# Kernel tuning notes

Measured on AMD Instinct MI355X. Metric: run time of the kernel, lower is better.

The kernel has to match this reference:

```python
import jax, jax.numpy as jnp
import numpy as np

B, T, L, W = 4, 4096, 64, 8          # batch, text len, media tokens, max_window_per_audio
DIM, DIM_A, H, DH = 2048, 1024, 8, 64
INNER = H * DH
LN_EPS = 1e-5


def setup_inputs() -> dict:
    key = jax.random.key(0)
    ks = jax.random.split(key, 8)
    x = jax.random.normal(ks[0], (B, T, DIM), jnp.float32)
    media = jax.random.normal(ks[1], (B, L, 1, DIM_A), jnp.float32)
    media_mask = jax.random.uniform(ks[2], (B, L, 1)) > 0.1
    # sparse media markers (~8 per row); ensure at least one per row
    media_locations = (jax.random.uniform(ks[3], (B, T)) < (8.0 / T)).astype(jnp.int32)
    media_locations = media_locations.at[:, 0].set(1)
    Wq = jax.random.normal(ks[4], (DIM, INNER), jnp.float32) / np.sqrt(DIM).astype(np.float32)
    Wkv = jax.random.normal(ks[5], (DIM_A, 2 * INNER), jnp.float32) / np.sqrt(DIM_A).astype(np.float32)
    Wout = jax.random.normal(ks[6], (INNER, DIM), jnp.float32) / np.sqrt(INNER).astype(np.float32)
    gamma = jnp.ones((DIM,), jnp.float32)
    beta = jnp.zeros((DIM,), jnp.float32)
    return dict(x=x, media=media, media_mask=media_mask, media_locations=media_locations,
                Wq=Wq, Wkv=Wkv, Wout=Wout, gamma=gamma, beta=beta)


def reference(x, media, media_mask, media_locations, Wq, Wkv, Wout, gamma, beta):
    scale = DH ** -0.5
    # LayerNorm (biased variance, like torch)
    mu = x.mean(-1, keepdims=True)
    var = x.var(-1, keepdims=True)
    xn = (x - mu) * jax.lax.rsqrt(var + LN_EPS) * gamma + beta
    # projections
    q = (xn @ Wq).reshape(B, T, H, DH).transpose(0, 2, 1, 3) * scale   # [B,h,T,dh]
    kv = media.reshape(B, L, DIM_A) @ Wkv
    k, v = jnp.split(kv, 2, axis=-1)
    k = k.reshape(B, L, H, DH).transpose(0, 2, 1, 3)                   # [B,h,L,dh]
    v = v.reshape(B, L, H, DH).transpose(0, 2, 1, 3)
    sim = jnp.einsum('bhid,bhjd->bhij', q, k)                          # [B,h,T,L]
    big = jnp.finfo(sim.dtype).max
    # media validity mask
    mm = media_mask.reshape(B, 1, 1, L)
    sim = jnp.where(mm, sim, -big)
    # few-shot window mask (only_attend_immediate_media=False):
    # token t attends windows [0, max(#media at <=t, 1) * W)
    cum = jnp.cumsum((media_locations != 0).astype(jnp.int32), axis=1)  # [B,T]
    end = jnp.maximum(cum, 1) * W                                       # [B,T]
    fsm = jnp.arange(L)[None, None, :] < end[:, :, None]                # [B,T,L]
    sim = jnp.where(fsm[:, None], sim, -big)
    sim = sim - jax.lax.stop_gradient(sim.max(-1, keepdims=True))
    attn = jax.nn.softmax(sim, axis=-1)
    out = jnp.einsum('bhij,bhjd->bhid', attn, v)                        # [B,h,T,dh]
    out = out.transpose(0, 2, 1, 3).reshape(B, T, INNER)
    return out @ Wout
```

## Files before the change

kernel.cpp:

```cpp
#include <hip/hip_runtime.h>
#include <float.h>

typedef __bf16 bf16;
typedef __bf16 bf16x8 __attribute__((ext_vector_type(8)));
typedef float f32x4 __attribute__((ext_vector_type(4)));
typedef float f32x16 __attribute__((ext_vector_type(16)));

#define GAS __attribute__((address_space(1)))
#define LAS __attribute__((address_space(3)))

__device__ __forceinline__ void gload_lds16(const void* g, void* l) {
  __builtin_amdgcn_global_load_lds((const GAS unsigned int*)g, (LAS unsigned int*)l, 16, 0, 0);
}

template <int OUT_BF16>
__global__ __launch_bounds__(512, 2) void gemm_big(
    const bf16* __restrict__ A, const bf16* __restrict__ Bt,
    void* __restrict__ Cv, int M, int N, int K) {
  __shared__ __align__(16) bf16 Abuf[3][256 * 64];
  __shared__ __align__(16) bf16 Bbuf[3][128 * 64];
  const int tid = threadIdx.x, lane = tid & 63;
  const int w = tid >> 6, wr = w >> 2, wc = w & 3;
  const int l31 = lane & 31, hi = lane >> 5;

  const int gx = gridDim.x;
  const int nwg = gx * gridDim.y;
  int lid = blockIdx.y * gx + blockIdx.x;
  {
    const int qq = nwg >> 3, rr = nwg & 7;
    const int xcd = lid & 7, pos = lid >> 3;
    lid = (xcd < rr ? xcd * (qq + 1) : rr * (qq + 1) + (xcd - rr) * qq) + pos;
  }
  const int bx = lid % gx, by = lid / gx;
  const size_t m0 = (size_t)by * 256, n0 = (size_t)bx * 128;

  const int nt = K >> 6;
  const int srow = tid >> 3;
  const int sslot = tid & 7;

  f32x16 acc[4] = {};

  auto stage = [&](int t) {
    const int s = t % 3;
    const int kt = t << 6;
#pragma unroll
    for (int c = 0; c < 4; ++c) {
      const int r = c * 64 + srow;
      gload_lds16(A + (m0 + r) * (size_t)K + kt + ((sslot ^ (r & 7)) << 3),
                  &Abuf[s][c * 4096 + w * 512]);
    }
#pragma unroll
    for (int c = 0; c < 2; ++c) {
      const int r = c * 64 + srow;
      gload_lds16(Bt + (n0 + r) * (size_t)K + kt + ((sslot ^ (r & 7)) << 3),
                  &Bbuf[s][c * 4096 + w * 512]);
    }
  };

  auto rdA = [&](int s, int mi, int ks) {
    const int r = wr * 128 + mi * 32 + l31;
    return *(const bf16x8*)&Abuf[s][r * 64 + ((((ks << 1) | hi) ^ (r & 7)) << 3)];
  };
  auto rdB = [&](int s, int ks) {
    const int r = wc * 32 + l31;
    return *(const bf16x8*)&Bbuf[s][r * 64 + ((((ks << 1) | hi) ^ (r & 7)) << 3)];
  };

  auto compute = [&](int t) {
    const int s = t % 3;
    bf16x8 bv[4];
#pragma unroll
    for (int ks = 0; ks < 4; ++ks) bv[ks] = rdB(s, ks);
    __builtin_amdgcn_s_setprio(1);
#pragma unroll
    for (int ks = 0; ks < 4; ++ks)
#pragma unroll
      for (int mi = 0; mi < 4; ++mi) {
        const bf16x8 av = rdA(s, mi, ks);
        acc[mi] = __builtin_amdgcn_mfma_f32_32x32x16_bf16(av, bv[ks], acc[mi],
                                                          0, 0, 0);
      }
    __builtin_amdgcn_s_setprio(0);
  };

  stage(0);
  stage(1);

  for (int t = 0; t < nt - 1; ++t) {
    __builtin_amdgcn_sched_barrier(0);
    asm volatile("s_waitcnt vmcnt(6)" ::: "memory");
    __builtin_amdgcn_s_barrier();
    __builtin_amdgcn_sched_barrier(0);
    if (t + 2 < nt) stage(t + 2);
    compute(t);
  }
  __builtin_amdgcn_sched_barrier(0);
  asm volatile("s_waitcnt vmcnt(0)" ::: "memory");
  __builtin_amdgcn_s_barrier();
  __builtin_amdgcn_sched_barrier(0);
  compute(nt - 1);

#pragma unroll
  for (int mi = 0; mi < 4; ++mi)
#pragma unroll
    for (int rg = 0; rg < 16; ++rg) {
      const size_t row =
          m0 + wr * 128 + mi * 32 + (rg & 3) + ((rg >> 2) << 3) + (hi << 2);
      const size_t col = n0 + wc * 32 + l31;
      if (OUT_BF16)
        ((bf16*)Cv)[row * (size_t)N + col] = (bf16)acc[mi][rg];
      else
        ((float*)Cv)[row * (size_t)N + col] = acc[mi][rg];
    }
}

template <int OUT_BF16>
__global__ __launch_bounds__(256, 2) void gemm_bt(
    const bf16* __restrict__ A, const bf16* __restrict__ Bt,
    void* __restrict__ Cv, int M, int N, int K) {
  __shared__ bf16 As[128 * 32];
  __shared__ bf16 Bs[128 * 32];
  const int tid = threadIdx.x;
  const int lane = tid & 63, w = tid >> 6;
  const int wr = w >> 1, wc = w & 1;

  const int gx = gridDim.x;
  const int nwg = gx * gridDim.y;
  int lid = blockIdx.y * gx + blockIdx.x;
  {
    const int qq = nwg >> 3, rr = nwg & 7;
    const int xcd = lid & 7, pos = lid >> 3;
    lid = (xcd < rr ? xcd * (qq + 1) : rr * (qq + 1) + (xcd - rr) * qq) + pos;
  }
  const int bx = lid % gx, by = lid / gx;
  const size_t m0 = (size_t)by * 128, n0 = (size_t)bx * 128;

  const int srow = lane >> 2, sslot = lane & 3;
  const int g = lane >> 4, fr = lane & 15;

  f32x4 acc[4][4] = {};

  for (int kt = 0; kt < K; kt += 32) {
    __syncthreads();
#pragma unroll
    for (int j = 0; j < 2; ++j) {
      const int c = 2 * w + j;
      const int r = c * 16 + srow;
      const int ks = (sslot ^ (r & 3)) << 3;
      gload_lds16(A + (m0 + r) * K + kt + ks, &As[c * 512]);
      gload_lds16(Bt + (n0 + r) * K + kt + ks, &Bs[c * 512]);
    }
    __syncthreads();
    bf16x8 av[4], bv[4];
#pragma unroll
    for (int mi = 0; mi < 4; ++mi) {
      const int r = wr * 64 + mi * 16 + fr;
      av[mi] = *(const bf16x8*)&As[r * 32 + ((g ^ (r & 3)) << 3)];
    }
#pragma unroll
    for (int ni = 0; ni < 4; ++ni) {
      const int r = wc * 64 + ni * 16 + fr;
      bv[ni] = *(const bf16x8*)&Bs[r * 32 + ((g ^ (r & 3)) << 3)];
    }
#pragma unroll
    for (int mi = 0; mi < 4; ++mi)
#pragma unroll
      for (int ni = 0; ni < 4; ++ni)
        acc[mi][ni] = __builtin_amdgcn_mfma_f32_16x16x32_bf16(
            av[mi], bv[ni], acc[mi][ni], 0, 0, 0);
  }

#pragma unroll
  for (int mi = 0; mi < 4; ++mi)
#pragma unroll
    for (int ni = 0; ni < 4; ++ni)
#pragma unroll
      for (int rg = 0; rg < 4; ++rg) {
        const size_t row = m0 + wr * 64 + mi * 16 + g * 4 + rg;
        const size_t col = n0 + wc * 64 + ni * 16 + fr;
        if (OUT_BF16)
          ((bf16*)Cv)[row * (size_t)N + col] = (bf16)acc[mi][ni][rg];
        else
          ((float*)Cv)[row * (size_t)N + col] = acc[mi][ni][rg];
      }
}

__device__ __forceinline__ void transp64(const float* __restrict__ src,
                                         bf16* __restrict__ dst, int R, int C,
                                         float scale, int tile, float* lds) {
  const int tilesC = C >> 6;
  const int tr = tile / tilesC, tc = tile % tilesC;
  const int r0 = tr << 6, c0 = tc << 6;
  const int tid = threadIdx.x;
  const int lr = tid >> 6, lc = tid & 63;
#pragma unroll
  for (int j = 0; j < 16; ++j) {
    const int r = j * 4 + lr;
    lds[r * 65 + lc] = src[(size_t)(r0 + r) * C + c0 + lc];
  }
  __syncthreads();
#pragma unroll
  for (int j = 0; j < 16; ++j) {
    const int rr = j * 4 + lr;
    dst[(size_t)(c0 + rr) * R + r0 + lc] = (bf16)(lds[lc * 65 + rr] * scale);
  }
}

__global__ __launch_bounds__(256) void prep_all(
    const float* __restrict__ x, const float* __restrict__ gamma,
    const float* __restrict__ beta, bf16* __restrict__ xn,
    const float* __restrict__ Wq, bf16* __restrict__ wqT,
    const float* __restrict__ Wkv, bf16* __restrict__ wkvT,
    const float* __restrict__ Wout, bf16* __restrict__ woT,
    const float* __restrict__ media, bf16* __restrict__ medb,
    const int* __restrict__ mloc, int* __restrict__ endw,
    const unsigned char* __restrict__ mraw, int* __restrict__ mk) {
  __shared__ float shf[64 * 65];
  const int blk = blockIdx.x, tid = threadIdx.x;

  if (blk < 16384) {
    const size_t base = (size_t)blk * 2048 + tid * 8;
    f32x4 v0 = *(const f32x4*)(x + base);
    f32x4 v1 = *(const f32x4*)(x + base + 4);
    float s = 0.f, q2 = 0.f;
#pragma unroll
    for (int j = 0; j < 4; ++j) {
      s += v0[j] + v1[j];
      q2 += v0[j] * v0[j] + v1[j] * v1[j];
    }
    for (int off = 32; off > 0; off >>= 1) {
      s += __shfl_down(s, off);
      q2 += __shfl_down(q2, off);
    }
    const int lane = tid & 63, wv = tid >> 6;
    if (lane == 0) { shf[wv] = s; shf[4 + wv] = q2; }
    __syncthreads();
    s = shf[0] + shf[1] + shf[2] + shf[3];
    q2 = shf[4] + shf[5] + shf[6] + shf[7];
    const float mu = s * (1.f / 2048.f);
    const float var = q2 * (1.f / 2048.f) - mu * mu;
    const float rs = rsqrtf(var + 1e-5f);
    f32x4 g0 = *(const f32x4*)(gamma + tid * 8);
    f32x4 g1 = *(const f32x4*)(gamma + tid * 8 + 4);
    f32x4 b0 = *(const f32x4*)(beta + tid * 8);
    f32x4 b1 = *(const f32x4*)(beta + tid * 8 + 4);
    bf16x8 o;
#pragma unroll
    for (int j = 0; j < 4; ++j) {
      o[j] = (bf16)((v0[j] - mu) * rs * g0[j] + b0[j]);
      o[4 + j] = (bf16)((v1[j] - mu) * rs * g1[j] + b1[j]);
    }
    *(bf16x8*)(xn + base) = o;
  } else if (blk < 16640) {
    transp64(Wq, wqT, 2048, 512, 0.125f, blk - 16384, shf);
  } else if (blk < 16896) {
    transp64(Wkv, wkvT, 1024, 1024, 1.f, blk - 16640, shf);
  } else if (blk < 17152) {
    transp64(Wout, woT, 512, 2048, 1.f, blk - 16896, shf);
  } else if (blk < 18176) {
    const int i = (blk - 17152) * 256 + tid;
    medb[i] = (bf16)media[i];
  } else if (blk < 18180) {
    int* part = (int*)shf;
    const int b = blk - 18176;
    int loc[16];
    int s = 0;
    const int base = b * 4096 + tid * 16;
#pragma unroll
    for (int j = 0; j < 16; ++j) {
      loc[j] = (mloc[base + j] != 0) ? 1 : 0;
      s += loc[j];
    }
    part[tid] = s;
    __syncthreads();
    for (int off = 1; off < 256; off <<= 1) {
      int v = (tid >= off) ? part[tid - off] : 0;
      __syncthreads();
      part[tid] += v;
      __syncthreads();
    }
    int c = (tid > 0) ? part[tid - 1] : 0;
#pragma unroll
    for (int j = 0; j < 16; ++j) {
      c += loc[j];
      int e = (c > 1 ? c : 1) << 3;
      endw[base + j] = e > 64 ? 64 : e;
    }
  } else {
    int* isbool = (int*)shf;
    if (tid == 0) *isbool = 0;
    __syncthreads();
    const unsigned char v = mraw[tid];
    if ((tid & 3) != 0 && v != 0) atomicOr(isbool, 1);
    __syncthreads();
    mk[tid] = (*isbool) ? (int)mraw[tid] : ((const int*)mraw)[tid];
  }
}

__global__ __launch_bounds__(256, 2) void attn_kernel(
    const bf16* __restrict__ q, const bf16* __restrict__ kv,
    const int* __restrict__ mk, const int* __restrict__ endw,
    bf16* __restrict__ ao) {
  __shared__ bf16 Ks[64 * 64], Vs[64 * 64], Ps[64 * 64];
  __shared__ int mks[64];
  const int tid = threadIdx.x, lane = tid & 63, w = tid >> 6;
  const int b = blockIdx.z, h = blockIdx.y, t0 = blockIdx.x * 64;

#pragma unroll
  for (int s0 = 0; s0 < 2; ++s0) {
    const int sidx = s0 * 256 + tid;
    const int r = sidx >> 3, sl = sidx & 7;
    *(bf16x8*)&Ks[r * 64 + ((sl ^ (r & 7)) << 3)] =
        *(const bf16x8*)&kv[(size_t)(b * 64 + r) * 1024 + h * 64 + sl * 8];
    bf16x8 vv =
        *(const bf16x8*)&kv[(size_t)(b * 64 + r) * 1024 + 512 + h * 64 + sl * 8];
#pragma unroll
    for (int j = 0; j < 8; ++j) {
      const int dh = sl * 8 + j;
      Vs[dh * 64 + ((((r >> 3) ^ (dh & 7)) << 3) | (r & 7))] = vv[j];
    }
  }
  if (tid < 64) mks[tid] = mk[b * 64 + tid];
  __syncthreads();

  const int g = lane >> 4, fr = lane & 15;
  bf16x8 aq[2];
#pragma unroll
  for (int kg = 0; kg < 2; ++kg)
    aq[kg] = *(const bf16x8*)&q[(size_t)(b * 4096 + t0 + w * 16 + fr) * 512 +
                                h * 64 + kg * 32 + g * 8];
  f32x4 sacc[4] = {};
#pragma unroll
  for (int kg = 0; kg < 2; ++kg)
#pragma unroll
    for (int ni = 0; ni < 4; ++ni) {
      const int r = ni * 16 + fr;
      bf16x8 bk = *(const bf16x8*)&Ks[r * 64 + (((kg * 4 + g) ^ (r & 7)) << 3)];
      sacc[ni] = __builtin_amdgcn_mfma_f32_16x16x32_bf16(aq[kg], bk, sacc[ni],
                                                         0, 0, 0);
    }

  const int4 ev4 = *(const int4*)&endw[b * 4096 + t0 + w * 16 + g * 4];
  const int ev[4] = {ev4.x, ev4.y, ev4.z, ev4.w};
  float p[4][4];
#pragma unroll
  for (int ni = 0; ni < 4; ++ni) {
    const int l = ni * 16 + fr;
    const bool mv = (mks[l] != 0);
#pragma unroll
    for (int rg = 0; rg < 4; ++rg)
      p[ni][rg] = (mv && (l < ev[rg])) ? sacc[ni][rg] : -FLT_MAX;
  }
#pragma unroll
  for (int rg = 0; rg < 4; ++rg) {
    float m = fmaxf(fmaxf(p[0][rg], p[1][rg]), fmaxf(p[2][rg], p[3][rg]));
    m = fmaxf(m, __shfl_xor(m, 1));
    m = fmaxf(m, __shfl_xor(m, 2));
    m = fmaxf(m, __shfl_xor(m, 4));
    m = fmaxf(m, __shfl_xor(m, 8));
    float sum = 0.f;
#pragma unroll
    for (int ni = 0; ni < 4; ++ni) {
      p[ni][rg] = __expf(p[ni][rg] - m);
      sum += p[ni][rg];
    }
    sum += __shfl_xor(sum, 1);
    sum += __shfl_xor(sum, 2);
    sum += __shfl_xor(sum, 4);
    sum += __shfl_xor(sum, 8);
    const float inv = 1.f / sum;
#pragma unroll
    for (int ni = 0; ni < 4; ++ni) p[ni][rg] *= inv;
  }
#pragma unroll
  for (int ni = 0; ni < 4; ++ni) {
    const int l = ni * 16 + fr;
#pragma unroll
    for (int rg = 0; rg < 4; ++rg) {
      const int tr = w * 16 + g * 4 + rg;
      Ps[tr * 64 + ((((l >> 3) ^ (tr & 7)) << 3) | (l & 7))] = (bf16)p[ni][rg];
    }
  }
  __syncthreads();

  bf16x8 pa[2];
#pragma unroll
  for (int kg = 0; kg < 2; ++kg) {
    const int r = w * 16 + fr;
    pa[kg] = *(const bf16x8*)&Ps[r * 64 + (((kg * 4 + g) ^ (r & 7)) << 3)];
  }
  f32x4 oacc[4] = {};
#pragma unroll
  for (int kg = 0; kg < 2; ++kg)
#pragma unroll
    for (int ni = 0; ni < 4; ++ni) {
      const int r = ni * 16 + fr;
      bf16x8 bv = *(const bf16x8*)&Vs[r * 64 + (((kg * 4 + g) ^ (r & 7)) << 3)];
      oacc[ni] = __builtin_amdgcn_mfma_f32_16x16x32_bf16(pa[kg], bv, oacc[ni],
                                                         0, 0, 0);
    }
#pragma unroll
  for (int ni = 0; ni < 4; ++ni)
#pragma unroll
    for (int rg = 0; rg < 4; ++rg)
      ao[(size_t)(b * 4096 + t0 + w * 16 + g * 4 + rg) * 512 + h * 64 +
         ni * 16 + fr] = (bf16)oacc[ni][rg];
}

extern "C" void kernel_launch(void* const* d_in, const int* in_sizes, int n_in,
                              void* d_out, int out_size, void* d_ws,
                              size_t ws_size, hipStream_t stream) {
  const float* x = (const float*)d_in[0];
  const float* media = (const float*)d_in[1];
  const unsigned char* mraw = (const unsigned char*)d_in[2];
  const int* mloc = (const int*)d_in[3];
  const float* Wq = (const float*)d_in[4];
  const float* Wkv = (const float*)d_in[5];
  const float* Wout = (const float*)d_in[6];
  const float* gamma = (const float*)d_in[7];
  const float* beta = (const float*)d_in[8];
  float* out = (float*)d_out;

  bf16* xn = (bf16*)d_out;

  char* ws = (char*)d_ws;
  size_t off = 0;
  auto carve = [&](size_t bytes) {
    void* p = ws + off;
    off += (bytes + 255) & ~(size_t)255;
    return p;
  };
  bf16* qb = (bf16*)carve((size_t)16384 * 512 * 2);
  bf16* aob = (bf16*)carve((size_t)16384 * 512 * 2);
  bf16* kvb = (bf16*)carve((size_t)256 * 1024 * 2);
  bf16* wqT = (bf16*)carve((size_t)512 * 2048 * 2);
  bf16* wkvT = (bf16*)carve((size_t)1024 * 1024 * 2);
  bf16* woT = (bf16*)carve((size_t)2048 * 512 * 2);
  bf16* medb = (bf16*)carve((size_t)256 * 1024 * 2);
  int* endw = (int*)carve((size_t)4 * 4096 * 4);
  int* mk = (int*)carve(256 * 4);
  (void)ws_size;
  (void)in_sizes;
  (void)n_in;
  (void)out_size;

  prep_all<<<18181, 256, 0, stream>>>(x, gamma, beta, xn, Wq, wqT, Wkv, wkvT,
                                      Wout, woT, media, medb, mloc, endw, mraw,
                                      mk);

  gemm_bt<1><<<dim3(8, 2), 256, 0, stream>>>(medb, wkvT, kvb, 256, 1024, 1024);

  gemm_big<1><<<dim3(4, 64), 512, 0, stream>>>(xn, wqT, qb, 16384, 512, 2048);

  attn_kernel<<<dim3(64, 8, 4), 256, 0, stream>>>(qb, kvb, mk, endw, aob);

  gemm_big<0><<<dim3(16, 64), 512, 0, stream>>>(aob, woT, out, 16384, 2048,
                                                512);
}
```

Before: 184.8 us.

## Fuse Q projection GEMM with cross-attention into a single kernel

Replaces the separate Q-projection GEMM and attention kernel with one kernel. Each 256x128 Q tile, covering two heads, is computed with 16x16x32 MFMAs, written to LDS, and then used directly for QK^T, masked softmax and PV against K/V loaded into the reused staging buffers. This removes the round trip of the 16 MB Q buffer through global memory and one kernel launch. In exchange, the GEMM switches from 32x32 to 16x16 MFMA tiles and adds register and LDS pressure from the attention epilogue.

```diff
diff --git a/kernel.cpp b/kernel.cpp
--- a/kernel.cpp
+++ b/kernel.cpp
@@ -11,6 +11,241 @@
 
 __device__ __forceinline__ void gload_lds16(const void* g, void* l) {
   __builtin_amdgcn_global_load_lds((const GAS unsigned int*)g, (LAS unsigned int*)l, 16, 0, 0);
+}
+
+__global__ __launch_bounds__(512, 2) void qattn(
+    const bf16* __restrict__ xn, const bf16* __restrict__ wqT,
+    const bf16* __restrict__ kvb, const int* __restrict__ mk,
+    const int* __restrict__ endw, bf16* __restrict__ aob) {
+  constexpr int K = 2048;
+  __shared__ __align__(16) bf16 Abuf[3][256 * 64];
+  __shared__ __align__(16) bf16 Bbuf[3][128 * 64];
+  const int tid = threadIdx.x, lane = tid & 63;
+  const int w = tid >> 6, wr = w >> 1, wc = w & 1;
+  const int g = lane >> 4, fr = lane & 15;
+
+  const int gx = gridDim.x;
+  const int nwg = gx * gridDim.y;
+  int lid = blockIdx.y * gx + blockIdx.x;
+  {
+    const int qq = nwg >> 3, rr = nwg & 7;
+    const int xcd = lid & 7, pos = lid >> 3;
+    lid = (xcd < rr ? xcd * (qq + 1) : rr * (qq + 1) + (xcd - rr) * qq) + pos;
+  }
+  const int bx = lid % gx, by = lid / gx;
+  const size_t m0 = (size_t)by * 256;
+  const int n0 = bx * 128;
+
+  const int nt = K >> 6;
+  const int srow = tid >> 3, sslot = tid & 7;
+
+  f32x4 acc[4][4] = {};
+
+  auto stage = [&](int t) {
+    const int s = t % 3;
+    const int kt = t << 6;
+#pragma unroll
+    for (int c = 0; c < 4; ++c) {
+      const int r = c * 64 + srow;
+      gload_lds16(xn + (m0 + r) * (size_t)K + kt + ((sslot ^ (r & 7)) << 3),
+                  &Abuf[s][c * 4096 + w * 512]);
+    }
+#pragma unroll
+    for (int c = 0; c < 2; ++c) {
+      const int r = c * 64 + srow;
+      gload_lds16(wqT + (size_t)(n0 + r) * K + kt + ((sslot ^ (r & 7)) << 3),
+                  &Bbuf[s][c * 4096 + w * 512]);
+    }
+  };
+  auto rdA = [&](int s, int mi, int ks) {
+    const int r = wr * 64 + mi * 16 + fr;
+    return *(const bf16x8*)&Abuf[s][r * 64 + ((((ks << 2) | g) ^ (r & 7)) << 3)];
+  };
+  auto rdB = [&](int s, int ni, int ks) {
+    const int r = wc * 64 + ni * 16 + fr;
+    return *(const bf16x8*)&Bbuf[s][r * 64 + ((((ks << 2) | g) ^ (r & 7)) << 3)];
+  };
+  auto compute = [&](int t) {
+    const int s = t % 3;
+    bf16x8 bv[4][2];
+#pragma unroll
+    for (int ni = 0; ni < 4; ++ni)
+#pragma unroll
+      for (int ks = 0; ks < 2; ++ks) bv[ni][ks] = rdB(s, ni, ks);
+    __builtin_amdgcn_s_setprio(1);
+#pragma unroll
+    for (int mi = 0; mi < 4; ++mi)
+#pragma unroll
+      for (int ks = 0; ks < 2; ++ks) {
+        const bf16x8 av = rdA(s, mi, ks);
+#pragma unroll
+        for (int ni = 0; ni < 4; ++ni)
+          acc[mi][ni] = __builtin_amdgcn_mfma_f32_16x16x32_bf16(
+              av, bv[ni][ks], acc[mi][ni], 0, 0, 0);
+      }
+    __builtin_amdgcn_s_setprio(0);
+  };
+
+  stage(0);
+  stage(1);
+  for (int t = 0; t < nt - 1; ++t) {
+    __builtin_amdgcn_sched_barrier(0);
+    asm volatile("s_waitcnt vmcnt(6)" ::: "memory");
+    __builtin_amdgcn_s_barrier();
+    __builtin_amdgcn_sched_barrier(0);
+    if (t + 2 < nt) stage(t + 2);
+    compute(t);
+  }
+  __builtin_amdgcn_sched_barrier(0);
+  asm volatile("s_waitcnt vmcnt(0)" ::: "memory");
+  __builtin_amdgcn_s_barrier();
+  __builtin_amdgcn_sched_barrier(0);
+  compute(nt - 1);
+
+  __builtin_amdgcn_s_barrier();
+  __builtin_amdgcn_sched_barrier(0);
+
+  const int b = (int)(m0 >> 12);
+  bf16* QP = &Abuf[0][0] + w * 4096;
+  bf16* Klds = &Bbuf[0][0];
+  bf16* Vlds = &Bbuf[1][0];
+
+#pragma unroll
+  for (int mi = 0; mi < 4; ++mi)
+#pragma unroll
+    for (int ni = 0; ni < 4; ++ni)
+#pragma unroll
+      for (int rg = 0; rg < 4; ++rg) {
+        const int row = mi * 16 + g * 4 + rg, col = ni * 16 + fr;
+        QP[row * 64 + (((col >> 3) ^ (row & 7)) << 3) + (col & 7)] =
+            (bf16)acc[mi][ni][rg];
+      }
+
+#pragma unroll
+  for (int j = 0; j < 2; ++j) {
+    const int idx = j * 512 + tid;
+    const int head = idx >> 9, l = (idx >> 3) & 63, sl = idx & 7;
+    gload_lds16(kvb + (size_t)(b * 64 + l) * 1024 + (2 * bx + head) * 64 +
+                    ((sl ^ (l & 7)) << 3),
+                Klds + (j * 512 + w * 64) * 8);
+  }
+#pragma unroll
+  for (int j = 0; j < 2; ++j) {
+    const int idx = j * 512 + tid;
+    const int head = idx >> 9, l = (idx >> 3) & 63, sg = idx & 7;
+    bf16x8 vv = *(const bf16x8*)&kvb[(size_t)(b * 64 + l) * 1024 + 512 +
+                                     (2 * bx + head) * 64 + sg * 8];
+#pragma unroll
+    for (int e = 0; e < 8; ++e) {
+      const int dh = sg * 8 + e;
+      Vlds[head * 4096 + dh * 64 + (((l >> 3) ^ (dh & 7)) << 3) + (l & 7)] =
+          vv[e];
+    }
+  }
+  asm volatile("s_waitcnt vmcnt(0)" ::: "memory");
+  __syncthreads();
+
+  f32x4 sacc[4][4] = {};
+#pragma unroll
+  for (int ks = 0; ks < 2; ++ks) {
+    bf16x8 aq[4], bk[4];
+#pragma unroll
+    for (int mi = 0; mi < 4; ++mi) {
+      const int r = mi * 16 + fr;
+      aq[mi] = *(const bf16x8*)&QP[r * 64 + ((((ks << 2) | g) ^ (r & 7)) << 3)];
+    }
+#pragma unroll
+    for (int ni = 0; ni < 4; ++ni) {
+      const int l = ni * 16 + fr;
+      bk[ni] = *(const bf16x8*)&Klds[wc * 4096 + l * 64 +
+                                     ((((ks << 2) | g) ^ (l & 7)) << 3)];
+    }
+#pragma unroll
+    for (int mi = 0; mi < 4; ++mi)
+#pragma unroll
+      for (int ni = 0; ni < 4; ++ni)
+        sacc[mi][ni] = __builtin_amdgcn_mfma_f32_16x16x32_bf16(
+            aq[mi], bk[ni], sacc[mi][ni], 0, 0, 0);
+  }
+
+#pragma unroll
+  for (int mi = 0; mi < 4; ++mi) {
+    const int4 ev4 = *(const int4*)&endw[m0 + wr * 64 + mi * 16 + g * 4];
+    const int ev[4] = {ev4.x, ev4.y, ev4.z, ev4.w};
+    float p[4][4];
+#pragma unroll
+    for (int ni = 0; ni < 4; ++ni) {
+      const int l = ni * 16 + fr;
+      const bool mv = (mk[b * 64 + l] != 0);
+#pragma unroll
+      for (int rg = 0; rg < 4; ++rg)
+        p[ni][rg] = (mv && (l < ev[rg])) ? sacc[mi][ni][rg] : -FLT_MAX;
+    }
+#pragma unroll
+    for (int rg = 0; rg < 4; ++rg) {
+      float m = fmaxf(fmaxf(p[0][rg], p[1][rg]), fmaxf(p[2][rg], p[3][rg]));
+      m = fmaxf(m, __shfl_xor(m, 1));
+      m = fmaxf(m, __shfl_xor(m, 2));
+      m = fmaxf(m, __shfl_xor(m, 4));
+      m = fmaxf(m, __shfl_xor(m, 8));
+      float sum = 0.f;
+#pragma unroll
+      for (int ni = 0; ni < 4; ++ni) {
+        p[ni][rg] = __expf(p[ni][rg] - m);
+        sum += p[ni][rg];
+      }
+      sum += __shfl_xor(sum, 1);
+      sum += __shfl_xor(sum, 2);
+      sum += __shfl_xor(sum, 4);
+      sum += __shfl_xor(sum, 8);
+      const float inv = 1.f / sum;
+#pragma unroll
+      for (int ni = 0; ni < 4; ++ni) p[ni][rg] *= inv;
+    }
+#pragma unroll
+    for (int ni = 0; ni < 4; ++ni) {
+      const int l = ni * 16 + fr;
+#pragma unroll
+      for (int rg = 0; rg < 4; ++rg) {
+        const int row = mi * 16 + g * 4 + rg;
+        QP[row * 64 + (((l >> 3) ^ (row & 7)) << 3) + (l & 7)] =
+            (bf16)p[ni][rg];
+      }
+    }
+  }
+
+  f32x4 oacc[4][4] = {};
+#pragma unroll
+  for (int ks = 0; ks < 2; ++ks) {
+    bf16x8 pa[4], bv[4];
+#pragma unroll
+    for (int mi = 0; mi < 4; ++mi) {
+      const int r = mi * 16 + fr;
+      pa[mi] = *(const bf16x8*)&QP[r * 64 + ((((ks << 2) | g) ^ (r & 7)) << 3)];
+    }
+#pragma unroll
+    for (int nd = 0; nd < 4; ++nd) {
+      const int dh = nd * 16 + fr;
+      bv[nd] = *(const bf16x8*)&Vlds[wc * 4096 + dh * 64 +
+                                     ((((ks << 2) | g) ^ (dh & 7)) << 3)];
+    }
+#pragma unroll
+    for (int mi = 0; mi < 4; ++mi)
+#pragma unroll
+      for (int nd = 0; nd < 4; ++nd)
+        oacc[mi][nd] = __builtin_amdgcn_mfma_f32_16x16x32_bf16(
+            pa[mi], bv[nd], oacc[mi][nd], 0, 0, 0);
+  }
+#pragma unroll
+  for (int mi = 0; mi < 4; ++mi)
+#pragma unroll
+    for (int nd = 0; nd < 4; ++nd)
+#pragma unroll
+      for (int rg = 0; rg < 4; ++rg) {
+        const size_t t = m0 + wr * 64 + mi * 16 + g * 4 + rg;
+        aob[t * 512 + (2 * bx + wc) * 64 + nd * 16 + fr] =
+            (bf16)oacc[mi][nd][rg];
+      }
 }
 
 template <int OUT_BF16>
@@ -85,7 +320,6 @@
 
   stage(0);
   stage(1);
-
   for (int t = 0; t < nt - 1; ++t) {
     __builtin_amdgcn_sched_barrier(0);
     asm volatile("s_waitcnt vmcnt(6)" ::: "memory");
@@ -297,116 +531,6 @@
   }
 }
 
-__global__ __launch_bounds__(256, 2) void attn_kernel(
-    const bf16* __restrict__ q, const bf16* __restrict__ kv,
-    const int* __restrict__ mk, const int* __restrict__ endw,
-    bf16* __restrict__ ao) {
-  __shared__ bf16 Ks[64 * 64], Vs[64 * 64], Ps[64 * 64];
-  __shared__ int mks[64];
-  const int tid = threadIdx.x, lane = tid & 63, w = tid >> 6;
-  const int b = blockIdx.z, h = blockIdx.y, t0 = blockIdx.x * 64;
-
-#pragma unroll
-  for (int s0 = 0; s0 < 2; ++s0) {
-    const int sidx = s0 * 256 + tid;
-    const int r = sidx >> 3, sl = sidx & 7;
-    *(bf16x8*)&Ks[r * 64 + ((sl ^ (r & 7)) << 3)] =
-        *(const bf16x8*)&kv[(size_t)(b * 64 + r) * 1024 + h * 64 + sl * 8];
-    bf16x8 vv =
-        *(const bf16x8*)&kv[(size_t)(b * 64 + r) * 1024 + 512 + h * 64 + sl * 8];
-#pragma unroll
-    for (int j = 0; j < 8; ++j) {
-      const int dh = sl * 8 + j;
-      Vs[dh * 64 + ((((r >> 3) ^ (dh & 7)) << 3) | (r & 7))] = vv[j];
-    }
-  }
-  if (tid < 64) mks[tid] = mk[b * 64 + tid];
-  __syncthreads();
-
-  const int g = lane >> 4, fr = lane & 15;
-  bf16x8 aq[2];
-#pragma unroll
-  for (int kg = 0; kg < 2; ++kg)
-    aq[kg] = *(const bf16x8*)&q[(size_t)(b * 4096 + t0 + w * 16 + fr) * 512 +
-                                h * 64 + kg * 32 + g * 8];
-  f32x4 sacc[4] = {};
-#pragma unroll
-  for (int kg = 0; kg < 2; ++kg)
-#pragma unroll
-    for (int ni = 0; ni < 4; ++ni) {
-      const int r = ni * 16 + fr;
-      bf16x8 bk = *(const bf16x8*)&Ks[r * 64 + (((kg * 4 + g) ^ (r & 7)) << 3)];
-      sacc[ni] = __builtin_amdgcn_mfma_f32_16x16x32_bf16(aq[kg], bk, sacc[ni],
-                                                         0, 0, 0);
-    }
-
-  const int4 ev4 = *(const int4*)&endw[b * 4096 + t0 + w * 16 + g * 4];
-  const int ev[4] = {ev4.x, ev4.y, ev4.z, ev4.w};
-  float p[4][4];
-#pragma unroll
-  for (int ni = 0; ni < 4; ++ni) {
-    const int l = ni * 16 + fr;
-    const bool mv = (mks[l] != 0);
-#pragma unroll
-    for (int rg = 0; rg < 4; ++rg)
-      p[ni][rg] = (mv && (l < ev[rg])) ? sacc[ni][rg] : -FLT_MAX;
-  }
-#pragma unroll
-  for (int rg = 0; rg < 4; ++rg) {
-    float m = fmaxf(fmaxf(p[0][rg], p[1][rg]), fmaxf(p[2][rg], p[3][rg]));
-    m = fmaxf(m, __shfl_xor(m, 1));
-    m = fmaxf(m, __shfl_xor(m, 2));
-    m = fmaxf(m, __shfl_xor(m, 4));
-    m = fmaxf(m, __shfl_xor(m, 8));
-    float sum = 0.f;
-#pragma unroll
-    for (int ni = 0; ni < 4; ++ni) {
-      p[ni][rg] = __expf(p[ni][rg] - m);
-      sum += p[ni][rg];
-    }
-    sum += __shfl_xor(sum, 1);
-    sum += __shfl_xor(sum, 2);
-    sum += __shfl_xor(sum, 4);
-    sum += __shfl_xor(sum, 8);
-    const float inv = 1.f / sum;
-#pragma unroll
-    for (int ni = 0; ni < 4; ++ni) p[ni][rg] *= inv;
-  }
-#pragma unroll
-  for (int ni = 0; ni < 4; ++ni) {
-    const int l = ni * 16 + fr;
-#pragma unroll
-    for (int rg = 0; rg < 4; ++rg) {
-      const int tr = w * 16 + g * 4 + rg;
-      Ps[tr * 64 + ((((l >> 3) ^ (tr & 7)) << 3) | (l & 7))] = (bf16)p[ni][rg];
-    }
-  }
-  __syncthreads();
-
-  bf16x8 pa[2];
-#pragma unroll
-  for (int kg = 0; kg < 2; ++kg) {
-    const int r = w * 16 + fr;
-    pa[kg] = *(const bf16x8*)&Ps[r * 64 + (((kg * 4 + g) ^ (r & 7)) << 3)];
-  }
-  f32x4 oacc[4] = {};
-#pragma unroll
-  for (int kg = 0; kg < 2; ++kg)
-#pragma unroll
-    for (int ni = 0; ni < 4; ++ni) {
-      const int r = ni * 16 + fr;
-      bf16x8 bv = *(const bf16x8*)&Vs[r * 64 + (((kg * 4 + g) ^ (r & 7)) << 3)];
-      oacc[ni] = __builtin_amdgcn_mfma_f32_16x16x32_bf16(pa[kg], bv, oacc[ni],
-                                                         0, 0, 0);
-    }
-#pragma unroll
-  for (int ni = 0; ni < 4; ++ni)
-#pragma unroll
-    for (int rg = 0; rg < 4; ++rg)
-      ao[(size_t)(b * 4096 + t0 + w * 16 + g * 4 + rg) * 512 + h * 64 +
-         ni * 16 + fr] = (bf16)oacc[ni][rg];
-}
-
 extern "C" void kernel_launch(void* const* d_in, const int* in_sizes, int n_in,
                               void* d_out, int out_size, void* d_ws,
                               size_t ws_size, hipStream_t stream) {
@@ -430,7 +554,6 @@
     off += (bytes + 255) & ~(size_t)255;
     return p;
   };
-  bf16* qb = (bf16*)carve((size_t)16384 * 512 * 2);
   bf16* aob = (bf16*)carve((size_t)16384 * 512 * 2);
   bf16* kvb = (bf16*)carve((size_t)256 * 1024 * 2);
   bf16* wqT = (bf16*)carve((size_t)512 * 2048 * 2);
@@ -450,9 +573,7 @@
 
   gemm_bt<1><<<dim3(8, 2), 256, 0, stream>>>(medb, wkvT, kvb, 256, 1024, 1024);
 
-  gemm_big<1><<<dim3(4, 64), 512, 0, stream>>>(xn, wqT, qb, 16384, 512, 2048);
-
-  attn_kernel<<<dim3(64, 8, 4), 256, 0, stream>>>(qb, kvb, mk, endw, aob);
+  qattn<<<dim3(4, 64), 512, 0, stream>>>(xn, wqT, kvb, mk, endw, aob);
 
   gemm_big<0><<<dim3(16, 64), 512, 0, stream>>>(aob, woT, out, 16384, 2048,
                                                 512);
```

After: 177.7 us. 3.8% less time.
